# Kernel tuning notes

Measured on AMD Instinct MI355X. Metric: run time of the kernel, lower is better.

## Reference

```python
import jax, jax.numpy as jnp
import numpy as np

N_NODES = 40000
N_EDGES = 640000
IN_FEATS = 128
HID = 64
# layer widths per GCN.__init__: in->h->2h->2h->h->h->h->1
DIMS = [IN_FEATS, HID, 2 * HID, 2 * HID, HID, HID, HID, 1]


def setup_inputs() -> dict:
    key = jax.random.key(0)
    ks = jax.random.split(key, 3 + 2 * 7)
    inp = {
        "in_feat": jax.random.normal(ks[0], (N_NODES, IN_FEATS), dtype=jnp.float32),
        "src": jax.random.randint(ks[1], (N_EDGES,), 0, N_NODES, dtype=jnp.int32),
        "dst": jax.random.randint(ks[2], (N_EDGES,), 0, N_NODES, dtype=jnp.int32),
    }
    # DGL GraphConv params: weight [in, out] (glorot), bias [out] (zeros; use small randn for a nontrivial baseline)
    for i in range(7):
        din, dout = DIMS[i], DIMS[i + 1]
        scale = jnp.sqrt(6.0 / (din + dout)).astype(jnp.float32)
        inp[f"W{i+1}"] = jax.random.uniform(ks[3 + 2 * i], (din, dout), jnp.float32, -scale, scale)
        inp[f"b{i+1}"] = 0.01 * jax.random.normal(ks[4 + 2 * i], (dout,), dtype=jnp.float32)
    return inp


def _graph_conv(x, W, b, src, dst, out_norm, in_norm, n_nodes):
    # DGL GraphConv, norm='both', allow_zero_in_degree=True:
    #   h = D_in^{-1/2} * A^T * (D_out^{-1/2} * x) @ W + b
    x = x * out_norm[:, None]
    if x.shape[1] > W.shape[1]:
        # mult W first to shrink message dim (mirrors DGL's heuristic; math-equivalent)
        x = x @ W
        h = jax.ops.segment_sum(x[src], dst, num_segments=n_nodes)
    else:
        h = jax.ops.segment_sum(x[src], dst, num_segments=n_nodes)
        h = h @ W
    return h * in_norm[:, None] + b


def reference(in_feat, src, dst, W1, b1, W2, b2, W3, b3, W4, b4, W5, b5, W6, b6, W7, b7):
    n = in_feat.shape[0]
    ones = jnp.ones((src.shape[0],), dtype=jnp.float32)
    out_deg = jax.ops.segment_sum(ones, src, num_segments=n)
    in_deg = jax.ops.segment_sum(ones, dst, num_segments=n)
    out_norm = jnp.where(out_deg > 0, jax.lax.rsqrt(jnp.maximum(out_deg, 1.0)), 0.0)
    in_norm = jnp.where(in_deg > 0, jax.lax.rsqrt(jnp.maximum(in_deg, 1.0)), 0.0)

    params = [(W1, b1), (W2, b2), (W3, b3), (W4, b4), (W5, b5), (W6, b6), (W7, b7)]
    h = in_feat
    for i, (W, b) in enumerate(params):
        h = _graph_conv(h, W, b, src, dst, out_norm, in_norm, n)
        if i < 6:
            h = jax.nn.relu(h)
    return h  # [N, 1]
```

## Files before the change

### kernel.cpp

```cpp
#include <hip/hip_runtime.h>
#include <hip/hip_bf16.h>


#define IN_F 128
#define NSLICE 60
#define SHB 13
#define NSHARD 5

typedef __attribute__((ext_vector_type(8))) short short8v;
typedef __attribute__((ext_vector_type(4))) float f32x4;
typedef __attribute__((ext_vector_type(8))) _Float16 half8v;

static __device__ __forceinline__ unsigned short f2bf(float x) {
    unsigned u = __builtin_bit_cast(unsigned, x);
    unsigned r = (u + 0x7FFFu + ((u >> 16) & 1u)) >> 16;
    return (unsigned short)r;
}
static __device__ __forceinline__ float bf2f(unsigned short h) {
    unsigned u = ((unsigned)h) << 16;
    return __builtin_bit_cast(float, u);
}


struct WDesc { const float* w; unsigned short* th; unsigned short* tl; int K; int N; int cum; };
struct WPack { WDesc d[6]; int total; };


__global__ __launch_bounds__(256) void prep_kernel(const int* __restrict__ src,
                                                   const int* __restrict__ dst,
                                                   int* __restrict__ scratch,
                                                   WPack p, int E) {
    constexpr int SH = 1 << SHB;
    __shared__ int h[SH];
    const int t = threadIdx.x;
    const int b = blockIdx.x;
    const int s = blockIdx.y;
    const int z = blockIdx.z;
    if (z == 2) {
        int i = (b + NSLICE * s) * 256 + t;
        if (i >= p.total) return;
        int wi = 0;
#pragma unroll
        for (int q = 1; q < 6; ++q) if (i >= p.d[q].cum) wi = q;
        WDesc d = p.d[wi];
        int local = i - d.cum;
        int k = local / d.N, n = local - k * d.N;
        float v = d.w[local];
        unsigned short hh = f2bf(v);
        d.th[(size_t)n * d.K + k] = hh;
        d.tl[(size_t)n * d.K + k] = f2bf(v - bf2f(hh));
        return;
    }
    const int* idx = z ? dst : src;
    for (int i = t; i < SH; i += 256) h[i] = 0;
    __syncthreads();
    const int per = (E + NSLICE - 1) / NSLICE;
    const int lo = b * per;
    const int hiE = min(lo + per, E);
    const int base = s << SHB;
    for (int e = lo + t; e < hiE; e += 256) {
        unsigned a = (unsigned)(idx[e] - base);
        if (a < (unsigned)SH) atomicAdd(&h[a], 1);
    }
    __syncthreads();
    int* so = scratch + ((size_t)((z * NSHARD + s) * NSLICE + b) << SHB);
    for (int i = t; i < SH; i += 256) so[i] = h[i];
}


__global__ __launch_bounds__(256) void hist_reduce_blk(
    const int* __restrict__ scratch, int* __restrict__ in_deg,
    float* __restrict__ out_nrm, float* __restrict__ in_nrm,
    int* __restrict__ blockSums) {
    constexpr int SH = 1 << SHB;
    __shared__ int ws4[4];
    const int t = threadIdx.x;
    const int base = blockIdx.x * 1024 + t * 4;
    const int s = base >> SHB;
    const int i = base & (SH - 1);
    int od[4] = {0, 0, 0, 0}, id[4] = {0, 0, 0, 0};
    const int* po = scratch + (((size_t)s * NSLICE) << SHB) + i;
    const int* pi = scratch + (((size_t)(NSHARD + s) * NSLICE) << SHB) + i;
    for (int b = 0; b < NSLICE; ++b) {
        int4 o4 = *reinterpret_cast<const int4*>(po + ((size_t)b << SHB));
        int4 i4 = *reinterpret_cast<const int4*>(pi + ((size_t)b << SHB));
        od[0] += o4.x; od[1] += o4.y; od[2] += o4.z; od[3] += o4.w;
        id[0] += i4.x; id[1] += i4.y; id[2] += i4.z; id[3] += i4.w;
    }
    *reinterpret_cast<int4*>(&in_deg[base]) = make_int4(id[0], id[1], id[2], id[3]);
    float4 onf, inf;
    onf.x = od[0] > 0 ? rsqrtf((float)od[0]) : 0.f;
    onf.y = od[1] > 0 ? rsqrtf((float)od[1]) : 0.f;
    onf.z = od[2] > 0 ? rsqrtf((float)od[2]) : 0.f;
    onf.w = od[3] > 0 ? rsqrtf((float)od[3]) : 0.f;
    inf.x = id[0] > 0 ? rsqrtf((float)id[0]) : 0.f;
    inf.y = id[1] > 0 ? rsqrtf((float)id[1]) : 0.f;
    inf.z = id[2] > 0 ? rsqrtf((float)id[2]) : 0.f;
    inf.w = id[3] > 0 ? rsqrtf((float)id[3]) : 0.f;
    *reinterpret_cast<float4*>(&out_nrm[base]) = onf;
    *reinterpret_cast<float4*>(&in_nrm[base]) = inf;
    int ssum = id[0] + id[1] + id[2] + id[3];
#pragma unroll
    for (int off = 32; off > 0; off >>= 1) ssum += __shfl_down(ssum, off);
    if ((t & 63) == 0) ws4[t >> 6] = ssum;
    __syncthreads();
    if (t == 0) blockSums[blockIdx.x] = ws4[0] + ws4[1] + ws4[2] + ws4[3];
}


__global__ __launch_bounds__(256) void scan_fill2(const int* __restrict__ deg,
                                                  const int* __restrict__ blockSums,
                                                  int* __restrict__ row_off,
                                                  int NBtop, int N, int E) {
    __shared__ int sOff;
    __shared__ int wtot[4];
    const int t = threadIdx.x;
    const int lane = t & 63;
    const int wid = t >> 6;
    if (wid == 0) {
        int v = (lane < NBtop && lane < blockIdx.x) ? blockSums[lane] : 0;
#pragma unroll
        for (int off = 32; off > 0; off >>= 1) v += __shfl_down(v, off);
        if (lane == 0) sOff = v;
    }
    const int base = blockIdx.x * 1024 + t * 4;
    int4 v = make_int4(0, 0, 0, 0);
    if (base + 3 < N) v = *reinterpret_cast<const int4*>(&deg[base]);
    else if (base < N) {
        v.x = deg[base];
        if (base + 1 < N) v.y = deg[base + 1];
        if (base + 2 < N) v.z = deg[base + 2];
    }
    const int s = v.x + v.y + v.z + v.w;
    int incl = s;
#pragma unroll
    for (int off = 1; off < 64; off <<= 1) {
        int u = __shfl_up(incl, off);
        if (lane >= off) incl += u;
    }
    if (lane == 63) wtot[wid] = incl;
    __syncthreads();
    int pre = sOff + incl - s;
    for (int i = 0; i < wid; ++i) pre += wtot[i];
    if (base < N) {
        int run = pre;
        row_off[base] = run; run += v.x;
        if (base + 1 < N) { row_off[base + 1] = run; run += v.y; }
        if (base + 2 < N) { row_off[base + 2] = run; run += v.z; }
        if (base + 3 < N) { row_off[base + 3] = run; }
    }
    if (blockIdx.x == 0 && t == 0) row_off[N] = E;
}

__global__ void slice_base_kernel(int* __restrict__ scratch,
                                  const int* __restrict__ row_off, int N) {
    constexpr int SH = 1 << SHB;
    int n = blockIdx.x * blockDim.x + threadIdx.x;
    if (n >= N) return;
    int s = n >> SHB;
    int i = n & (SH - 1);
    int run = row_off[n];
    for (int b = 0; b < NSLICE; ++b) {
        size_t off = ((size_t)((NSHARD + s) * NSLICE + b) << SHB) + i;
        int c = scratch[off];
        scratch[off] = run;
        run += c;
    }
}

__global__ __launch_bounds__(256) void fill2_kernel(const int* __restrict__ src,
                                                    const int* __restrict__ dst,
                                                    const int* __restrict__ scratch,
                                                    int* __restrict__ csr, int E) {
    constexpr int SH = 1 << SHB;
    __shared__ int cur[SH];
    const int t = threadIdx.x;
    const int b = blockIdx.x;
    const int s = blockIdx.y;
    const int* base = scratch + ((size_t)((NSHARD + s) * NSLICE + b) << SHB);
    for (int i = t; i < SH; i += 256) cur[i] = base[i];
    __syncthreads();
    const int per = (E + NSLICE - 1) / NSLICE;
    const int lo = b * per;
    const int hiE = min(lo + per, E);
    const int nb = s << SHB;
    for (int e = lo + t; e < hiE; e += 256) {
        unsigned a = (unsigned)(dst[e] - nb);
        if (a < (unsigned)SH) {
            int pos = atomicAdd(&cur[a], 1);
            csr[pos] = src[e];
        }
    }
}


template<int K, int NOUT>
__global__ __launch_bounds__(256) void gemm_mfma_f32(
    const float* __restrict__ X,
    const unsigned short* __restrict__ Bh, const unsigned short* __restrict__ Bl,
    const float* __restrict__ pre, _Float16* __restrict__ Y16, int M) {
    constexpr int NT = NOUT / 16;
    const int lane = threadIdx.x & 63;
    const int wv = threadIdx.x >> 6;
    const int r0 = blockIdx.x * 64 + wv * 16;
    const int arow = r0 + (lane & 15);
    const int kg = (lane >> 4) * 8;
    const float sc = pre[arow];

    f32x4 acc[NT];
#pragma unroll
    for (int n = 0; n < NT; ++n) acc[n] = (f32x4){0.f, 0.f, 0.f, 0.f};

    for (int kk = 0; kk < K; kk += 32) {
        const float* ap = &X[(size_t)arow * K + kk + kg];
        float4 v0 = *reinterpret_cast<const float4*>(ap);
        float4 v1 = *reinterpret_cast<const float4*>(ap + 4);
        float a[8] = {v0.x, v0.y, v0.z, v0.w, v1.x, v1.y, v1.z, v1.w};
        short8v a_h, a_l;
#pragma unroll
        for (int j = 0; j < 8; ++j) {
            float f = a[j] * sc;
            unsigned short hh = f2bf(f);
            a_h[j] = (short)hh;
            a_l[j] = (short)f2bf(f - bf2f(hh));
        }
#pragma unroll
        for (int n = 0; n < NT; ++n) {
            int col = n * 16 + (lane & 15);
            short8v b_h = *reinterpret_cast<const short8v*>(Bh + (size_t)col * K + kk + kg);
            short8v b_l = *reinterpret_cast<const short8v*>(Bl + (size_t)col * K + kk + kg);
            acc[n] = __builtin_amdgcn_mfma_f32_16x16x32_bf16(a_h, b_h, acc[n], 0, 0, 0);
            acc[n] = __builtin_amdgcn_mfma_f32_16x16x32_bf16(a_h, b_l, acc[n], 0, 0, 0);
            acc[n] = __builtin_amdgcn_mfma_f32_16x16x32_bf16(a_l, b_h, acc[n], 0, 0, 0);
        }
    }
    const int c0 = lane & 15;
    const int rr = r0 + (lane >> 4) * 4;
#pragma unroll
    for (int n = 0; n < NT; ++n) {
        const int col = n * 16 + c0;
#pragma unroll
        for (int j = 0; j < 4; ++j)
            Y16[(size_t)(rr + j) * NOUT + col] = (_Float16)acc[n][j];
    }
}


template<int K, int NOUT, bool EPI, bool GEMV7>
__global__ __launch_bounds__(256) void gemm_h16(
    const _Float16* __restrict__ X,
    const unsigned short* __restrict__ Bh, const unsigned short* __restrict__ Bl,
    const float* __restrict__ r_nrm, const float* __restrict__ s_nrm,
    const float* __restrict__ bias, const float* __restrict__ W7,
    _Float16* __restrict__ Y16, float* __restrict__ T7, int M) {
    constexpr int NT = NOUT / 16;
    const int lane = threadIdx.x & 63;
    const int wv = threadIdx.x >> 6;
    const int r0 = blockIdx.x * 64 + wv * 16;
    const int arow = r0 + (lane & 15);
    const int kg = (lane >> 4) * 8;

    f32x4 acc[NT];
#pragma unroll
    for (int n = 0; n < NT; ++n) acc[n] = (f32x4){0.f, 0.f, 0.f, 0.f};

    for (int kk = 0; kk < K; kk += 32) {
        half8v av = *reinterpret_cast<const half8v*>(&X[(size_t)arow * K + kk + kg]);
        short8v a_h, a_l;
#pragma unroll
        for (int j = 0; j < 8; ++j) {
            float f = (float)av[j];
            unsigned short hh = f2bf(f);
            a_h[j] = (short)hh;
            a_l[j] = (short)f2bf(f - bf2f(hh));
        }
#pragma unroll
        for (int n = 0; n < NT; ++n) {
            int col = n * 16 + (lane & 15);
            short8v b_h = *reinterpret_cast<const short8v*>(Bh + (size_t)col * K + kk + kg);
            short8v b_l = *reinterpret_cast<const short8v*>(Bl + (size_t)col * K + kk + kg);
            acc[n] = __builtin_amdgcn_mfma_f32_16x16x32_bf16(a_h, b_h, acc[n], 0, 0, 0);
            acc[n] = __builtin_amdgcn_mfma_f32_16x16x32_bf16(a_h, b_l, acc[n], 0, 0, 0);
            acc[n] = __builtin_amdgcn_mfma_f32_16x16x32_bf16(a_l, b_h, acc[n], 0, 0, 0);
        }
    }
    const int c0 = lane & 15;
    const int rr = r0 + (lane >> 4) * 4;
    if (GEMV7) {
        float w7c[NT];
#pragma unroll
        for (int n = 0; n < NT; ++n) w7c[n] = W7[n * 16 + c0];
#pragma unroll
        for (int j = 0; j < 4; ++j) {
            const int row = rr + j;
            const float rn = r_nrm[row];
            const float sn = s_nrm[row];
            float p = 0.f;
#pragma unroll
            for (int n = 0; n < NT; ++n) {
                float y = fmaf(acc[n][j], rn, bias[n * 16 + c0]);
                y = fmaxf(y, 0.f) * sn;
                p = fmaf(y, w7c[n], p);
            }
#pragma unroll
            for (int m = 8; m >= 1; m >>= 1) p += __shfl_xor(p, m);
            if (c0 == 0) T7[row] = p;
        }
    } else {
#pragma unroll
        for (int n = 0; n < NT; ++n) {
            const int col = n * 16 + c0;
            const float bcol = EPI ? bias[col] : 0.f;
#pragma unroll
            for (int j = 0; j < 4; ++j) {
                const int row = rr + j;
                float y = acc[n][j];
                if (EPI) {
                    y = fmaf(y, r_nrm[row], bcol);
                    y = fmaxf(y, 0.f);
                    y *= s_nrm[row];
                }
                Y16[(size_t)row * NOUT + col] = (_Float16)y;
            }
        }
    }
}


template<int F, bool EPI>
__global__ __launch_bounds__(256) void agg_h16(
    const _Float16* __restrict__ X, const int* __restrict__ csr,
    const int* __restrict__ row_off, const float* __restrict__ r_nrm,
    const float* __restrict__ s_nrm, const float* __restrict__ bias,
    _Float16* __restrict__ Y16, int N) {
    constexpr int LPE = F / 8;
    constexpr int EPW = 64 / LPE;
    const int lane = threadIdx.x & 63;
    const int node = blockIdx.x * (blockDim.x >> 6) + (threadIdx.x >> 6);
    if (node >= N) return;
    const int g = lane / LPE;
    const int c = lane % LPE;
    const int lo = row_off[node];
    const int hi = row_off[node + 1];
    float acc[8], acc2[8];
#pragma unroll
    for (int j = 0; j < 8; ++j) { acc[j] = 0.f; acc2[j] = 0.f; }
    int e = lo + g;
    for (; e + EPW < hi; e += 2 * EPW) {
        int s0 = csr[e];
        int s1 = csr[e + EPW];
        half8v x0 = *reinterpret_cast<const half8v*>(&X[(size_t)s0 * F + c * 8]);
        half8v x1 = *reinterpret_cast<const half8v*>(&X[(size_t)s1 * F + c * 8]);
#pragma unroll
        for (int j = 0; j < 8; ++j) { acc[j] += (float)x0[j]; acc2[j] += (float)x1[j]; }
    }
    if (e < hi) {
        int s0 = csr[e];
        half8v x0 = *reinterpret_cast<const half8v*>(&X[(size_t)s0 * F + c * 8]);
#pragma unroll
        for (int j = 0; j < 8; ++j) acc[j] += (float)x0[j];
    }
#pragma unroll
    for (int j = 0; j < 8; ++j) acc[j] += acc2[j];
#pragma unroll
    for (int m = LPE; m < 64; m <<= 1) {
#pragma unroll
        for (int j = 0; j < 8; ++j) acc[j] += __shfl_xor(acc[j], m);
    }
    if (lane < LPE) {
        half8v o;
        if (EPI) {
            float rn = r_nrm[node];
            float sn = s_nrm[node];
#pragma unroll
            for (int j = 0; j < 8; ++j) {
                float y = fmaf(acc[j], rn, bias[lane * 8 + j]);
                o[j] = (_Float16)(fmaxf(y, 0.f) * sn);
            }
        } else {
#pragma unroll
            for (int j = 0; j < 8; ++j) o[j] = (_Float16)acc[j];
        }
        *reinterpret_cast<half8v*>(&Y16[(size_t)node * F + lane * 8]) = o;
    }
}


__global__ __launch_bounds__(256) void agg1_kernel(const float* __restrict__ T,
                                                   const int* __restrict__ csr,
                                                   const int* __restrict__ row_off,
                                                   const float* __restrict__ r_nrm,
                                                   const float* __restrict__ bias,
                                                   float* __restrict__ Y, int N) {
    const int node = blockIdx.x * 16 + (threadIdx.x >> 4);
    const int l = threadIdx.x & 15;
    if (node >= N) return;
    const int lo = row_off[node];
    const int hi = row_off[node + 1];
    float acc = 0.f;
    for (int e = lo + l; e < hi; e += 16) acc += T[csr[e]];
#pragma unroll
    for (int m = 8; m >= 1; m >>= 1) acc += __shfl_xor(acc, m);
    if (l == 0) Y[node] = fmaf(acc, r_nrm[node], bias[0]);
}


extern "C" void kernel_launch(void* const* d_in, const int* in_sizes, int n_in,
                              void* d_out, int out_size, void* d_ws, size_t ws_size,
                              hipStream_t stream) {
    const float* in_feat = (const float*)d_in[0];
    const int* src = (const int*)d_in[1];
    const int* dst = (const int*)d_in[2];
    const float* W1 = (const float*)d_in[3];  const float* B1 = (const float*)d_in[4];
    const float* W2 = (const float*)d_in[5];  const float* B2 = (const float*)d_in[6];
    const float* W3 = (const float*)d_in[7];  const float* B3 = (const float*)d_in[8];
    const float* W4 = (const float*)d_in[9];  const float* B4 = (const float*)d_in[10];
    const float* W5 = (const float*)d_in[11]; const float* B5 = (const float*)d_in[12];
    const float* W6 = (const float*)d_in[13]; const float* B6 = (const float*)d_in[14];
    const float* W7 = (const float*)d_in[15]; const float* B7 = (const float*)d_in[16];

    const int N = in_sizes[0] / IN_F;
    const int E = in_sizes[1];
    const int N2 = NSHARD << SHB;
    float* out = (float*)d_out;

    char* w = (char*)d_ws;
    auto alloc = [&](size_t bytes) { char* p = w; w += (bytes + 255) & ~(size_t)255; return p; };
    int* csr      = (int*)alloc((size_t)E * 4);
    int* row_off  = (int*)alloc((size_t)(N + 1) * 4);
    int* in_deg   = (int*)alloc((size_t)N2 * 4);
    int* blockSums= (int*)alloc(64 * 4);
    float* out_nrm= (float*)alloc((size_t)N2 * 4);
    float* in_nrm = (float*)alloc((size_t)N2 * 4);
    float* t7     = (float*)alloc((size_t)N * 4);
    const int dims[8] = {128, 64, 128, 128, 64, 64, 64, 1};
    unsigned short* wth[6]; unsigned short* wtl[6];
    for (int i = 0; i < 6; ++i) {
        size_t kn = (size_t)dims[i] * dims[i + 1];
        wth[i] = (unsigned short*)alloc(kn * 2);
        wtl[i] = (unsigned short*)alloc(kn * 2);
    }
    _Float16* h0 = (_Float16*)alloc((size_t)N * 128 * 2);
    _Float16* h1 = (_Float16*)alloc((size_t)N * 128 * 2);
    int* scratch = (int*)h0;
    (void)ws_size; (void)n_in; (void)out_size;

    const int TB = 256;
    const int NB = N2 / 1024;

    WPack wp;
    const float* Ws[6] = {W1, W2, W3, W4, W5, W6};
    int cum = 0;
    for (int i = 0; i < 6; ++i) {
        wp.d[i] = {Ws[i], wth[i], wtl[i], dims[i], dims[i + 1], cum};
        cum += dims[i] * dims[i + 1];
    }
    wp.total = cum;

    prep_kernel<<<dim3(NSLICE, NSHARD, 3), TB, 0, stream>>>(src, dst, scratch, wp, E);
    hist_reduce_blk<<<NB, TB, 0, stream>>>(scratch, in_deg, out_nrm, in_nrm, blockSums);
    scan_fill2<<<NB, TB, 0, stream>>>(in_deg, blockSums, row_off, NB, N, E);
    slice_base_kernel<<<(N + TB - 1) / TB, TB, 0, stream>>>(scratch, row_off, N);
    fill2_kernel<<<dim3(NSLICE, NSHARD), TB, 0, stream>>>(src, dst, scratch, csr, E);

    const int gridN4 = (N + 3) / 4;
    const int MB = (N + 63) / 64;

    gemm_mfma_f32<128, 64><<<MB, TB, 0, stream>>>(in_feat, wth[0], wtl[0], out_nrm, h0, N);
    agg_h16<64, true><<<gridN4, TB, 0, stream>>>(h0, csr, row_off, in_nrm, out_nrm, B1, h1, N);

    agg_h16<64, false><<<gridN4, TB, 0, stream>>>(h1, csr, row_off, nullptr, nullptr, nullptr, h0, N);
    gemm_h16<64, 128, true, false><<<MB, TB, 0, stream>>>(
        h0, wth[1], wtl[1], in_nrm, out_nrm, B2, nullptr, h1, nullptr, N);

    agg_h16<128, false><<<gridN4, TB, 0, stream>>>(h1, csr, row_off, nullptr, nullptr, nullptr, h0, N);
    gemm_h16<128, 128, true, false><<<MB, TB, 0, stream>>>(
        h0, wth[2], wtl[2], in_nrm, out_nrm, B3, nullptr, h1, nullptr, N);

    gemm_h16<128, 64, false, false><<<MB, TB, 0, stream>>>(
        h1, wth[3], wtl[3], nullptr, nullptr, nullptr, nullptr, h0, nullptr, N);
    agg_h16<64, true><<<gridN4, TB, 0, stream>>>(h0, csr, row_off, in_nrm, out_nrm, B4, h1, N);

    agg_h16<64, false><<<gridN4, TB, 0, stream>>>(h1, csr, row_off, nullptr, nullptr, nullptr, h0, N);
    gemm_h16<64, 64, true, false><<<MB, TB, 0, stream>>>(
        h0, wth[4], wtl[4], in_nrm, out_nrm, B5, nullptr, h1, nullptr, N);

    agg_h16<64, false><<<gridN4, TB, 0, stream>>>(h1, csr, row_off, nullptr, nullptr, nullptr, h0, N);
    gemm_h16<64, 64, true, true><<<MB, TB, 0, stream>>>(
        h0, wth[5], wtl[5], in_nrm, out_nrm, B6, W7, nullptr, t7, N);

    agg1_kernel<<<(N + 15) / 16, TB, 0, stream>>>(t7, csr, row_off, in_nrm, B7, out, N);
}
```

Before: 294.5 us.

## Fuse slice-base prefix into scan kernel and unroll aggregation loop by four

Merges the per-slice base computation into the row-offset scan kernel, so each thread walks its four nodes' slice counters with int4 loads and stores. This removes one kernel launch and the reread of row_off. The neighbour-gather loop in agg_h16 now issues four independent row loads per iteration instead of two, giving more memory-level parallelism, with a per-edge tail loop for leftovers. The fused scan only handles nodes when base+3<N, which is safe only because the node count is padded to a multiple of four.

Result: no change. 298.5 us (+1.4%).

```diff
diff --git a/kernel.cpp b/kernel.cpp
--- a/kernel.cpp
+++ b/kernel.cpp
@@ -108,10 +108,12 @@
 }
 
 
-__global__ __launch_bounds__(256) void scan_fill2(const int* __restrict__ deg,
-                                                  const int* __restrict__ blockSums,
-                                                  int* __restrict__ row_off,
-                                                  int NBtop, int N, int E) {
+__global__ __launch_bounds__(256) void scanslice_kernel(const int* __restrict__ deg,
+                                                        const int* __restrict__ blockSums,
+                                                        int* __restrict__ row_off,
+                                                        int* __restrict__ scratch,
+                                                        int NBtop, int N, int E) {
+    constexpr int SH = 1 << SHB;
     __shared__ int sOff;
     __shared__ int wtot[4];
     const int t = threadIdx.x;
@@ -131,8 +133,8 @@
         if (base + 1 < N) v.y = deg[base + 1];
         if (base + 2 < N) v.z = deg[base + 2];
     }
-    const int s = v.x + v.y + v.z + v.w;
-    int incl = s;
+    const int s4 = v.x + v.y + v.z + v.w;
+    int incl = s4;
 #pragma unroll
     for (int off = 1; off < 64; off <<= 1) {
         int u = __shfl_up(incl, off);
@@ -140,32 +142,25 @@
     }
     if (lane == 63) wtot[wid] = incl;
     __syncthreads();
-    int pre = sOff + incl - s;
+    int pre = sOff + incl - s4;
     for (int i = 0; i < wid; ++i) pre += wtot[i];
-    if (base < N) {
-        int run = pre;
-        row_off[base] = run; run += v.x;
-        if (base + 1 < N) { row_off[base + 1] = run; run += v.y; }
-        if (base + 2 < N) { row_off[base + 2] = run; run += v.z; }
-        if (base + 3 < N) { row_off[base + 3] = run; }
+    if (base + 3 < N) {
+        int runs0 = pre;
+        int runs1 = runs0 + v.x;
+        int runs2 = runs1 + v.y;
+        int runs3 = runs2 + v.z;
+        *reinterpret_cast<int4*>(&row_off[base]) = make_int4(runs0, runs1, runs2, runs3);
+        const int s = base >> SHB;
+        const int i = base & (SH - 1);
+        int4 run = make_int4(runs0, runs1, runs2, runs3);
+        for (int b = 0; b < NSLICE; ++b) {
+            size_t off = ((size_t)((NSHARD + s) * NSLICE + b) << SHB) + i;
+            int4 c4 = *reinterpret_cast<const int4*>(&scratch[off]);
+            *reinterpret_cast<int4*>(&scratch[off]) = run;
+            run.x += c4.x; run.y += c4.y; run.z += c4.z; run.w += c4.w;
+        }
     }
     if (blockIdx.x == 0 && t == 0) row_off[N] = E;
-}
-
-__global__ void slice_base_kernel(int* __restrict__ scratch,
-                                  const int* __restrict__ row_off, int N) {
-    constexpr int SH = 1 << SHB;
-    int n = blockIdx.x * blockDim.x + threadIdx.x;
-    if (n >= N) return;
-    int s = n >> SHB;
-    int i = n & (SH - 1);
-    int run = row_off[n];
-    for (int b = 0; b < NSLICE; ++b) {
-        size_t off = ((size_t)((NSHARD + s) * NSLICE + b) << SHB) + i;
-        int c = scratch[off];
-        scratch[off] = run;
-        run += c;
-    }
 }
 
 __global__ __launch_bounds__(256) void fill2_kernel(const int* __restrict__ src,
@@ -346,15 +341,22 @@
 #pragma unroll
     for (int j = 0; j < 8; ++j) { acc[j] = 0.f; acc2[j] = 0.f; }
     int e = lo + g;
-    for (; e + EPW < hi; e += 2 * EPW) {
+    for (; e + 3 * EPW < hi; e += 4 * EPW) {
         int s0 = csr[e];
         int s1 = csr[e + EPW];
+        int s2 = csr[e + 2 * EPW];
+        int s3 = csr[e + 3 * EPW];
         half8v x0 = *reinterpret_cast<const half8v*>(&X[(size_t)s0 * F + c * 8]);
         half8v x1 = *reinterpret_cast<const half8v*>(&X[(size_t)s1 * F + c * 8]);
-#pragma unroll
-        for (int j = 0; j < 8; ++j) { acc[j] += (float)x0[j]; acc2[j] += (float)x1[j]; }
-    }
-    if (e < hi) {
+        half8v x2 = *reinterpret_cast<const half8v*>(&X[(size_t)s2 * F + c * 8]);
+        half8v x3 = *reinterpret_cast<const half8v*>(&X[(size_t)s3 * F + c * 8]);
+#pragma unroll
+        for (int j = 0; j < 8; ++j) {
+            acc[j] += (float)x0[j] + (float)x2[j];
+            acc2[j] += (float)x1[j] + (float)x3[j];
+        }
+    }
+    for (; e < hi; e += EPW) {
         int s0 = csr[e];
         half8v x0 = *reinterpret_cast<const half8v*>(&X[(size_t)s0 * F + c * 8]);
 #pragma unroll
@@ -459,8 +461,7 @@
 
     prep_kernel<<<dim3(NSLICE, NSHARD, 3), TB, 0, stream>>>(src, dst, scratch, wp, E);
     hist_reduce_blk<<<NB, TB, 0, stream>>>(scratch, in_deg, out_nrm, in_nrm, blockSums);
-    scan_fill2<<<NB, TB, 0, stream>>>(in_deg, blockSums, row_off, NB, N, E);
-    slice_base_kernel<<<(N + TB - 1) / TB, TB, 0, stream>>>(scratch, row_off, N);
+    scanslice_kernel<<<NB, TB, 0, stream>>>(in_deg, blockSums, row_off, scratch, NB, N, E);
     fill2_kernel<<<dim3(NSLICE, NSHARD), TB, 0, stream>>>(src, dst, scratch, csr, E);
 
     const int gridN4 = (N + 3) / 4;
```
